# Optimization experiments

Hardware: AMD Instinct MI355X
Metric: run time of the kernel (lower is better)

Reference implementation:

```python
import jax, jax.numpy as jnp
import numpy as np

LN_EPS = 1e-5


def setup_inputs() -> dict:
    key = jax.random.key(0)
    k1, k2, k3 = jax.random.split(key, 3)
    N, IN_DIM, D_MODEL, B = 1_000_000, 128, 128, 1024
    node_emb = jax.random.normal(k1, (N, IN_DIM), dtype=jnp.float32)
    batch_idx = jnp.sort(jax.random.randint(k2, (N,), 0, B, dtype=jnp.int32))
    # Linear params (kaiming-uniform-ish scale), LayerNorm affine params
    scale = 1.0 / np.sqrt(IN_DIM)
    W = jax.random.uniform(k3, (IN_DIM, D_MODEL), dtype=jnp.float32, minval=-scale, maxval=scale)
    b = jnp.zeros((D_MODEL,), dtype=jnp.float32)
    gamma = jnp.ones((D_MODEL,), dtype=jnp.float32)
    beta = jnp.zeros((D_MODEL,), dtype=jnp.float32)
    return {"node_emb": node_emb, "batch_idx": batch_idx, "batch_size": B,
            "W": W, "b": b, "gamma": gamma, "beta": beta}


def reference(node_emb, batch_idx, batch_size, W, b, gamma, beta):
    # Linear -> GELU (exact erf, torch default) -> Dropout (eval: identity) -> LayerNorm
    h = jax.nn.gelu(node_emb @ W + b, approximate=False)
    mu = jnp.mean(h, axis=-1, keepdims=True)
    var = jnp.mean((h - mu) ** 2, axis=-1, keepdims=True)
    node_proj = (h - mu) * jax.lax.rsqrt(var + LN_EPS) * gamma + beta  # [N, D]

    N = node_proj.shape[0]
    counts = jnp.bincount(batch_idx, length=batch_size)          # [B] nodes per graph
    starts = jnp.cumsum(counts) - counts                          # group start offsets
    pos = jnp.arange(N) - starts[batch_idx]                       # within-graph position
    T = int(jnp.max(counts))                                      # padded token length

    # Single scatter into padded [B, T, D] buffer (replaces split + pad_sequence)
    tokens = jnp.zeros((batch_size, T, node_proj.shape[1]), dtype=node_proj.dtype)
    tokens = tokens.at[batch_idx, pos].set(node_proj)
    enc_mask = (jnp.arange(T)[None, :] < counts[:, None]).astype(jnp.int32)  # [B, T]
    return tokens, enc_mask
```

## Files before the change

kernel.cpp:

```cpp
#include <hip/hip_runtime.h>
#include <hip/hip_bf16.h>


#define NDIM 128

typedef __attribute__((ext_vector_type(8))) short bf16x8;
typedef __attribute__((ext_vector_type(4))) float f32x4;

__device__ __forceinline__ short f2bf(float f) {
    return __builtin_bit_cast(short, __float2bfloat16(f));
}

__global__ void starts_kernel(const int* __restrict__ bidx, int N, int B,
                              int* __restrict__ starts) {
    int b = blockIdx.x * blockDim.x + threadIdx.x;
    if (b > B) return;
    int lo = 0, hi = N;
    while (lo < hi) {
        int mid = (lo + hi) >> 1;
        if (bidx[mid] < b) lo = mid + 1; else hi = mid;
    }
    starts[b] = lo;
}

__global__ __launch_bounds__(256) void pad_mask_kernel(
    const int* __restrict__ starts, float* __restrict__ out, int T, int B) {
    const int b = blockIdx.x;
    const int cnt = starts[b + 1] - starts[b];
    float* mask = out + (size_t)B * T * NDIM + (size_t)b * T;
    for (int t = threadIdx.x; t < T; t += blockDim.x)
        mask[t] = (t < cnt) ? 1.0f : 0.0f;
    float4* pad = reinterpret_cast<float4*>(out + ((size_t)b * T + cnt) * NDIM);
    const int n4 = (T - cnt) * (NDIM / 4);
    float4 z = make_float4(0.f, 0.f, 0.f, 0.f);
    for (int i = threadIdx.x; i < n4; i += blockDim.x) pad[i] = z;
}


#define LOADX(BUF, TT)                                                        \
    do {                                                                      \
        int tc_ = (TT);                                                       \
        if (tc_ >= ntiles) tc_ = ntiles - 1;                                  \
        const float* xp_ = X + (size_t)(tc_ * 16 + m) * NDIM + g * 8;         \
        BUF[0] = *reinterpret_cast<const f32x4*>(xp_);                        \
        BUF[1] = *reinterpret_cast<const f32x4*>(xp_ + 4);                    \
        BUF[2] = *reinterpret_cast<const f32x4*>(xp_ + 32);                   \
        BUF[3] = *reinterpret_cast<const f32x4*>(xp_ + 36);                   \
        BUF[4] = *reinterpret_cast<const f32x4*>(xp_ + 64);                   \
        BUF[5] = *reinterpret_cast<const f32x4*>(xp_ + 68);                   \
        BUF[6] = *reinterpret_cast<const f32x4*>(xp_ + 96);                   \
        BUF[7] = *reinterpret_cast<const f32x4*>(xp_ + 100);                  \
    } while (0)

#define PROCESS(BUF, OBUF, TCUR, TPF)                                         \
    do {                                                                      \
        const int tcur_ = (TCUR);                                             \
        LOADX(OBUF, (TPF));                                                   \
        asm volatile("" ::: "memory");          \
        f32x4 acc[8];                                                         \
        _Pragma("unroll") for (int nt = 0; nt < 8; ++nt)                      \
            acc[nt] = (f32x4){0.f, 0.f, 0.f, 0.f};                            \
        _Pragma("unroll") for (int ks = 0; ks < 4; ++ks) {                    \
            bf16x8 aks;                                                       \
            _Pragma("unroll") for (int j = 0; j < 4; ++j) {                   \
                aks[j] = f2bf(BUF[2 * ks][j]);                                \
                aks[4 + j] = f2bf(BUF[2 * ks + 1][j]);                        \
            }                                                                 \
            _Pragma("unroll") for (int nt = 0; nt < 8; ++nt) {                \
                bf16x8 bf = *reinterpret_cast<const bf16x8*>(                 \
                    &wlds[((nt * 4 + ks) * 64 + lane) * 8]);                  \
                acc[nt] = __builtin_amdgcn_mfma_f32_16x16x32_bf16(            \
                    aks, bf, acc[nt], 0, 0, 0);                               \
            }                                                                 \
        }                                                                     \
                                                        \
        _Pragma("unroll") for (int nt = 0; nt < 8; ++nt) {                    \
            _Pragma("unroll") for (int r = 0; r < 4; ++r) {                   \
                float v = acc[nt][r] + bv[nt];                                \
                float q = v * v;                                              \
                float t1 = fmaf(q, 0.044715f, 1.0f);                          \
                float u = v * t1 * -1.5957691216f;                            \
                float e = __expf(u);                                          \
                acc[nt][r] = __fdividef(v, 1.0f + e);                         \
            }                                                                 \
        }                                                                     \
                                        \
        _Pragma("unroll") for (int r = 0; r < 4; ++r) {                       \
            float s = 0.f, sq = 0.f;                                          \
            _Pragma("unroll") for (int nt = 0; nt < 8; ++nt) {                \
                float v = acc[nt][r];                                         \
                s += v;                                                       \
                sq += v * v;                                                  \
            }                                                                 \
            _Pragma("unroll") for (int off = 1; off < 16; off <<= 1) {        \
                s += __shfl_xor(s, off, 64);                                  \
                sq += __shfl_xor(sq, off, 64);                                \
            }                                                                 \
            float mu = s * (1.0f / 128.0f);                                   \
            float var = sq * (1.0f / 128.0f) - mu * mu;                       \
            float rstd = rsqrtf(var + 1e-5f);                                 \
            _Pragma("unroll") for (int nt = 0; nt < 8; ++nt)                  \
                acc[nt][r] = (acc[nt][r] - mu) * rstd * gv[nt] + btv[nt];     \
        }                                                                     \
                                                  \
        const int myrow_ = tcur_ * 16 + m;                                    \
        const int myb_ = bidx[myrow_];                                        \
        const int myorow_ = myb_ * T + (myrow_ - starts[myb_]);               \
        _Pragma("unroll") for (int r = 0; r < 4; ++r) {                       \
            int orow = __shfl(myorow_, g * 4 + r, 64);                        \
            float* op = tokens + (size_t)orow * NDIM + m;                     \
            _Pragma("unroll") for (int nt = 0; nt < 8; ++nt)                  \
                op[nt * 16] = acc[nt][r];                                     \
        }                                                                     \
    } while (0)

__global__ __launch_bounds__(256, 3) void fused_kernel(
    const float* __restrict__ X, const int* __restrict__ bidx,
    const float* __restrict__ W, const float* __restrict__ bias,
    const float* __restrict__ gamma, const float* __restrict__ beta,
    const int* __restrict__ starts, float* __restrict__ tokens,
    int ntiles, int T) {
    __shared__ short wlds[16384];

    const int tid = threadIdx.x;
    const int lane = tid & 63;
    const int wave = tid >> 6;
    const int g = lane >> 4;
    const int m = lane & 15;

#pragma unroll
    for (int i = 0; i < 8; ++i) {
        int s = i * 256 + tid;
        int lane_s = s & 63;
        int fi = s >> 6;
        int gs = lane_s >> 4, ms = lane_s & 15;
        int nts = fi >> 2, kss = fi & 3;
        const float* wp = W + (size_t)(kss * 32 + gs * 8) * NDIM + nts * 16 + ms;
        bf16x8 f;
#pragma unroll
        for (int j = 0; j < 8; ++j) f[j] = f2bf(wp[(size_t)j * NDIM]);
        *reinterpret_cast<bf16x8*>(&wlds[s * 8]) = f;
    }

    float bv[8], gv[8], btv[8];
#pragma unroll
    for (int nt = 0; nt < 8; ++nt) {
        int c = nt * 16 + m;
        bv[nt] = bias[c];
        gv[nt] = gamma[c];
        btv[nt] = beta[c];
    }
    __syncthreads();

    const int nwaves = gridDim.x * 4;
    const int wave_gid = blockIdx.x * 4 + wave;

    f32x4 bufA[8], bufB[8];
    int t = wave_gid;
    LOADX(bufA, t);
    while (true) {
        PROCESS(bufA, bufB, t, t + nwaves);
        t += nwaves;
        if (t >= ntiles) break;
        PROCESS(bufB, bufA, t, t + nwaves);
        t += nwaves;
        if (t >= ntiles) break;
    }
}

extern "C" void kernel_launch(void* const* d_in, const int* in_sizes, int n_in,
                              void* d_out, int out_size, void* d_ws, size_t ws_size,
                              hipStream_t stream) {
    const float* X     = (const float*)d_in[0];
    const int*   bidx  = (const int*)d_in[1];
    const float* W     = (const float*)d_in[3];
    const float* bias  = (const float*)d_in[4];
    const float* gamma = (const float*)d_in[5];
    const float* beta  = (const float*)d_in[6];
    float* out = (float*)d_out;

    const int B = 1024;
    const int N = in_sizes[0] / NDIM;
    const int T = out_size / (B * (NDIM + 1));

    int* starts = (int*)d_ws;

    starts_kernel<<<dim3((B + 1 + 255) / 256), dim3(256), 0, stream>>>(bidx, N, B, starts);

    pad_mask_kernel<<<dim3(B), dim3(256), 0, stream>>>(starts, out, T, B);

    const int ntiles = N / 16;
    const int nblocks = 768;
    fused_kernel<<<dim3(nblocks), dim3(256), 0, stream>>>(
        X, bidx, W, bias, gamma, beta, starts, out, ntiles, T);
}
```

Measured before the change: 243.3 us.

## Deepen X prefetch to two tiles and fold pad/mask fill into fused kernel

The fused kernel now keeps two tiles of X in flight: each buffer is converted to bf16 first, then reloaded with the tile two steps ahead. This hides more global-load latency at the cost of extra live registers. The bidx/starts lookup is hoisted to the start of each tile so its latency overlaps with compute. The separate pad/mask kernel is removed, and its zero-fill and mask writes run at the tail of the fused kernel, which saves one launch but serializes that work after the main loop.

```diff
diff --git a/kernel.cpp b/kernel.cpp
--- a/kernel.cpp
+++ b/kernel.cpp
@@ -23,54 +23,50 @@
     starts[b] = lo;
 }
 
-__global__ __launch_bounds__(256) void pad_mask_kernel(
-    const int* __restrict__ starts, float* __restrict__ out, int T, int B) {
-    const int b = blockIdx.x;
-    const int cnt = starts[b + 1] - starts[b];
-    float* mask = out + (size_t)B * T * NDIM + (size_t)b * T;
-    for (int t = threadIdx.x; t < T; t += blockDim.x)
-        mask[t] = (t < cnt) ? 1.0f : 0.0f;
-    float4* pad = reinterpret_cast<float4*>(out + ((size_t)b * T + cnt) * NDIM);
-    const int n4 = (T - cnt) * (NDIM / 4);
-    float4 z = make_float4(0.f, 0.f, 0.f, 0.f);
-    for (int i = threadIdx.x; i < n4; i += blockDim.x) pad[i] = z;
-}
-
 
 #define LOADX(BUF, TT)                                                        \
     do {                                                                      \
-        int tc_ = (TT);                                                       \
-        if (tc_ >= ntiles) tc_ = ntiles - 1;                                  \
-        const float* xp_ = X + (size_t)(tc_ * 16 + m) * NDIM + g * 8;         \
-        BUF[0] = *reinterpret_cast<const f32x4*>(xp_);                        \
-        BUF[1] = *reinterpret_cast<const f32x4*>(xp_ + 4);                    \
-        BUF[2] = *reinterpret_cast<const f32x4*>(xp_ + 32);                   \
-        BUF[3] = *reinterpret_cast<const f32x4*>(xp_ + 36);                   \
-        BUF[4] = *reinterpret_cast<const f32x4*>(xp_ + 64);                   \
-        BUF[5] = *reinterpret_cast<const f32x4*>(xp_ + 68);                   \
-        BUF[6] = *reinterpret_cast<const f32x4*>(xp_ + 96);                   \
-        BUF[7] = *reinterpret_cast<const f32x4*>(xp_ + 100);                  \
+        const int tl_ = (TT);                                                 \
+        if (tl_ < ntiles) {                                                   \
+            const float* xp_ = X + (size_t)(tl_ * 16 + m) * NDIM + g * 8;     \
+            BUF[0] = *reinterpret_cast<const f32x4*>(xp_);                    \
+            BUF[1] = *reinterpret_cast<const f32x4*>(xp_ + 4);                \
+            BUF[2] = *reinterpret_cast<const f32x4*>(xp_ + 32);               \
+            BUF[3] = *reinterpret_cast<const f32x4*>(xp_ + 36);               \
+            BUF[4] = *reinterpret_cast<const f32x4*>(xp_ + 64);               \
+            BUF[5] = *reinterpret_cast<const f32x4*>(xp_ + 68);               \
+            BUF[6] = *reinterpret_cast<const f32x4*>(xp_ + 96);               \
+            BUF[7] = *reinterpret_cast<const f32x4*>(xp_ + 100);              \
+        }                                                                     \
     } while (0)
 
-#define PROCESS(BUF, OBUF, TCUR, TPF)                                         \
+#define PROCESS(BUF, TCUR, TPF)                                               \
     do {                                                                      \
         const int tcur_ = (TCUR);                                             \
-        LOADX(OBUF, (TPF));                                                   \
+                \
+        const int myrow_ = tcur_ * 16 + m;                                    \
+        const int myb_ = bidx[myrow_];                                        \
+        const int myorow_ = myb_ * T + (myrow_ - starts[myb_]);               \
+              \
+        bf16x8 a_[4];                                                         \
+        _Pragma("unroll") for (int ks = 0; ks < 4; ++ks) {                    \
+            _Pragma("unroll") for (int j = 0; j < 4; ++j) {                   \
+                a_[ks][j] = f2bf(BUF[2 * ks][j]);                             \
+                a_[ks][4 + j] = f2bf(BUF[2 * ks + 1][j]);                     \
+            }                                                                 \
+        }                                                                     \
+                        \
+        LOADX(BUF, (TPF));                                                    \
         asm volatile("" ::: "memory");          \
         f32x4 acc[8];                                                         \
         _Pragma("unroll") for (int nt = 0; nt < 8; ++nt)                      \
             acc[nt] = (f32x4){0.f, 0.f, 0.f, 0.f};                            \
         _Pragma("unroll") for (int ks = 0; ks < 4; ++ks) {                    \
-            bf16x8 aks;                                                       \
-            _Pragma("unroll") for (int j = 0; j < 4; ++j) {                   \
-                aks[j] = f2bf(BUF[2 * ks][j]);                                \
-                aks[4 + j] = f2bf(BUF[2 * ks + 1][j]);                        \
-            }                                                                 \
             _Pragma("unroll") for (int nt = 0; nt < 8; ++nt) {                \
                 bf16x8 bf = *reinterpret_cast<const bf16x8*>(                 \
                     &wlds[((nt * 4 + ks) * 64 + lane) * 8]);                  \
                 acc[nt] = __builtin_amdgcn_mfma_f32_16x16x32_bf16(            \
-                    aks, bf, acc[nt], 0, 0, 0);                               \
+                    a_[ks], bf, acc[nt], 0, 0, 0);                            \
             }                                                                 \
         }                                                                     \
                                                         \
@@ -103,9 +99,6 @@
                 acc[nt][r] = (acc[nt][r] - mu) * rstd * gv[nt] + btv[nt];     \
         }                                                                     \
                                                   \
-        const int myrow_ = tcur_ * 16 + m;                                    \
-        const int myb_ = bidx[myrow_];                                        \
-        const int myorow_ = myb_ * T + (myrow_ - starts[myb_]);               \
         _Pragma("unroll") for (int r = 0; r < 4; ++r) {                       \
             int orow = __shfl(myorow_, g * 4 + r, 64);                        \
             float* op = tokens + (size_t)orow * NDIM + m;                     \
@@ -119,7 +112,7 @@
     const float* __restrict__ W, const float* __restrict__ bias,
     const float* __restrict__ gamma, const float* __restrict__ beta,
     const int* __restrict__ starts, float* __restrict__ tokens,
-    int ntiles, int T) {
+    int ntiles, int T, int B) {
     __shared__ short wlds[16384];
 
     const int tid = threadIdx.x;
@@ -152,19 +145,31 @@
     }
     __syncthreads();
 
-    const int nwaves = gridDim.x * 4;
+    const int nw = gridDim.x * 4;
     const int wave_gid = blockIdx.x * 4 + wave;
 
     f32x4 bufA[8], bufB[8];
     int t = wave_gid;
     LOADX(bufA, t);
+    LOADX(bufB, t + nw);
     while (true) {
-        PROCESS(bufA, bufB, t, t + nwaves);
-        t += nwaves;
+        PROCESS(bufA, t, t + 2 * nw);
+        t += nw;
         if (t >= ntiles) break;
-        PROCESS(bufB, bufA, t, t + nwaves);
-        t += nwaves;
+        PROCESS(bufB, t, t + 2 * nw);
+        t += nw;
         if (t >= ntiles) break;
+    }
+
+    const float4 z4 = make_float4(0.f, 0.f, 0.f, 0.f);
+    for (int b = blockIdx.x; b < B; b += gridDim.x) {
+        const int cnt = starts[b + 1] - starts[b];
+        float* mask = tokens + (size_t)B * T * NDIM + (size_t)b * T;
+        for (int t2 = tid; t2 < T; t2 += 256)
+            mask[t2] = (t2 < cnt) ? 1.0f : 0.0f;
+        float4* pad = reinterpret_cast<float4*>(tokens + ((size_t)b * T + cnt) * NDIM);
+        const int n4 = (T - cnt) * (NDIM / 4);
+        for (int i = tid; i < n4; i += 256) pad[i] = z4;
     }
 }
 
@@ -187,10 +192,8 @@
 
     starts_kernel<<<dim3((B + 1 + 255) / 256), dim3(256), 0, stream>>>(bidx, N, B, starts);
 
-    pad_mask_kernel<<<dim3(B), dim3(256), 0, stream>>>(starts, out, T, B);
-
     const int ntiles = N / 16;
     const int nblocks = 768;
     fused_kernel<<<dim3(nblocks), dim3(256), 0, stream>>>(
-        X, bidx, W, bias, gamma, beta, starts, out, ntiles, T);
+        X, bidx, W, bias, gamma, beta, starts, out, ntiles, T, B);
 }
```

Measured after the change: 256.4 us. +5.4%, slower.
